# Optimization experiments

Hardware: AMD Instinct MI355X
Metric: run time of the kernel (lower is better)

The kernel has to match this reference:

```python
import jax, jax.numpy as jnp
import numpy as np
import math

NUM_HEADS = 16
TOPK = 64
EMBED = 1024

def setup_inputs() -> dict:
    key = jax.random.key(0)
    ks = jax.random.split(key, 11)
    b, s, e = 2, 2048, EMBED
    scale = 1.0 / math.sqrt(e)
    inp = {
        'q': jax.random.normal(ks[0], (b, s, e), dtype=jnp.float32),
        'k': jax.random.normal(ks[1], (b, s, e), dtype=jnp.float32),
        'v': jax.random.normal(ks[2], (b, s, e), dtype=jnp.float32),
        'Wq': jax.random.normal(ks[3], (e, e), dtype=jnp.float32) * scale,
        'bq': jnp.zeros((e,), dtype=jnp.float32),
        'Wk': jax.random.normal(ks[4], (e, e), dtype=jnp.float32) * scale,
        'bk': jnp.zeros((e,), dtype=jnp.float32),
        'Wv': jax.random.normal(ks[5], (e, e), dtype=jnp.float32) * scale,
        'bv': jnp.zeros((e,), dtype=jnp.float32),
        'Wo': jax.random.normal(ks[6], (e, e), dtype=jnp.float32) * scale,
        'bo': jnp.zeros((e,), dtype=jnp.float32),
    }
    return inp

def _topk_attention(Q, K, V, topk):
    # Q,K,V: (b, h, s, d)
    d = Q.shape[-1]
    scores = jnp.einsum('bhqd,bhkd->bhqk', Q, K) / jnp.sqrt(jnp.asarray(d, Q.dtype))
    topk_scores, topk_idx = jax.lax.top_k(scores, topk)  # (b,h,s,topk)
    probs = jax.nn.softmax(topk_scores, axis=-1)
    # gather V rows per (b,h): V_bh[idx] -> (s, topk, d); avoids (b,h,s,s,d) expand
    gather = jax.vmap(jax.vmap(lambda Vbh, idx: Vbh[idx]))
    sel = gather(V, topk_idx)  # (b,h,s,topk,d)
    return jnp.einsum('bhqk,bhqkd->bhqd', probs, sel)

def reference(q, k, v, Wq, bq, Wk, bk, Wv, bv, Wo, bo):
    b, s, e = q.shape
    h = NUM_HEADS
    d = e // h
    # NOTE: original torch code reshapes (b, s, e) -> (b, h, s, d) directly (no transpose)
    Q = (q @ Wq.T + bq).reshape(b, h, s, d)
    K = (k @ Wk.T + bk).reshape(b, h, s, d)
    V = (v @ Wv.T + bv).reshape(b, h, s, d)
    attn = _topk_attention(Q, K, V, TOPK)  # (b,h,s,d)
    out = attn.reshape(b, s, e)
    return out @ Wo.T + bo
```

## Files before the change

kernel.cpp:

```cpp
#include <hip/hip_runtime.h>
#include <stdint.h>

using u8  = unsigned char;
using s8  = signed char;
using u16 = unsigned short;
using u32 = unsigned int;
using u64 = unsigned long long;

typedef int   v4i __attribute__((ext_vector_type(4)));
typedef float v4f __attribute__((ext_vector_type(4)));
typedef short v8s __attribute__((ext_vector_type(8)));

__device__ __forceinline__ u16 f2bf(float f){
  u32 u = __builtin_bit_cast(u32, f);
  u32 r = (u + 0x7FFFu + ((u >> 16) & 1u)) >> 16;
  return (u16)r;
}
__device__ __forceinline__ float bf2f(u16 b){
  u32 u = ((u32)b) << 16;
  return __builtin_bit_cast(float, u);
}

__global__ __launch_bounds__(256) void quant_digits(
    const float* __restrict__ in, s8* __restrict__ dig, int n, float scale, float clampv)
{
  int t = blockIdx.x * 256 + threadIdx.x;
  int n8 = n >> 3;
  if (t >= n8) return;
  const float4* inv = (const float4*)in;
  float4 a = inv[2*t], b = inv[2*t+1];
  float xs[8] = {a.x,a.y,a.z,a.w,b.x,b.y,b.z,b.w};
  u64 p0=0,p1=0,p2=0,p3=0;
#pragma unroll
  for (int j=0;j<8;j++){
    float xv = fminf(fmaxf(xs[j], -clampv), clampv);
    int X = (int)rintf(xv * scale);
    int d0 = (int)(s8)(X & 255); X = (X - d0) >> 8;
    int d1 = (int)(s8)(X & 255); X = (X - d1) >> 8;
    int d2 = (int)(s8)(X & 255); X = (X - d2) >> 8;
    int d3 = X;
    p0 |= ((u64)(u8)(s8)d0) << (8*j);
    p1 |= ((u64)(u8)(s8)d1) << (8*j);
    p2 |= ((u64)(u8)(s8)d2) << (8*j);
    p3 |= ((u64)(u8)(s8)d3) << (8*j);
  }
  u64* o = (u64*)dig;
  size_t np8 = (size_t)n8;
  o[t] = p0; o[np8 + t] = p1; o[2*np8 + t] = p2; o[3*np8 + t] = p3;
}

#define MFMA_I8(c, a, b) asm volatile("v_mfma_i32_16x16x64_i8 %0, %1, %2, %0" : "+v"(c) : "v"(a), "v"(b))

__global__ __launch_bounds__(256) void gemm_i8(
    const s8* __restrict__ Ad, const s8* __restrict__ Wd, const float* __restrict__ bias,
    double* __restrict__ Cd, u16* __restrict__ Cb, u16* __restrict__ Cl)
{
  __shared__ alignas(16) s8 As[4][32][80];
  __shared__ alignas(16) s8 Bs[4][32][80];
  const int i0 = blockIdx.x * 32, o0 = blockIdx.y * 32;
  const int t = threadIdx.x, w = t >> 6, lane = t & 63;
  const int wr = w >> 1, wc = w & 1, l15 = lane & 15, lg = lane >> 4;
  const size_t APL = 4194304, WPL = 1048576;

  v4i c0={0,0,0,0}, c1={0,0,0,0}, c2={0,0,0,0}, c3={0,0,0,0}, c4={0,0,0,0};

  for (int kt = 0; kt < 16; ++kt){
#pragma unroll
    for (int j = 0; j < 2; ++j){
      int cid = t*2 + j;
      int p = cid >> 7, rem = cid & 127;
      int row = rem >> 2, c16 = (rem & 3) << 4;
      int4 av = *(const int4*)(Ad + (size_t)p*APL + (size_t)(i0+row)*1024 + kt*64 + c16);
      *(int4*)&As[p][row][c16] = av;
      int4 bv = *(const int4*)(Wd + (size_t)p*WPL + (size_t)(o0+row)*1024 + kt*64 + c16);
      *(int4*)&Bs[p][row][c16] = bv;
    }
    __syncthreads();
    v4i a0 = *(const v4i*)&As[0][wr*16+l15][lg*16];
    v4i a1 = *(const v4i*)&As[1][wr*16+l15][lg*16];
    v4i a2 = *(const v4i*)&As[2][wr*16+l15][lg*16];
    v4i a3 = *(const v4i*)&As[3][wr*16+l15][lg*16];
    v4i b0 = *(const v4i*)&Bs[0][wc*16+l15][lg*16];
    v4i b1 = *(const v4i*)&Bs[1][wc*16+l15][lg*16];
    v4i b2 = *(const v4i*)&Bs[2][wc*16+l15][lg*16];
    v4i b3 = *(const v4i*)&Bs[3][wc*16+l15][lg*16];
    MFMA_I8(c0, a0, b2); MFMA_I8(c0, a1, b1); MFMA_I8(c0, a2, b0);
    MFMA_I8(c1, a0, b3); MFMA_I8(c1, a1, b2); MFMA_I8(c1, a2, b1); MFMA_I8(c1, a3, b0);
    MFMA_I8(c2, a1, b3); MFMA_I8(c2, a2, b2); MFMA_I8(c2, a3, b1);
    MFMA_I8(c3, a2, b3); MFMA_I8(c3, a3, b2);
    MFMA_I8(c4, a3, b3);
    __syncthreads();
  }
  const int oc = o0 + wc*16 + l15;
  const double bv = (double)bias[oc];
#pragma unroll
  for (int e = 0; e < 4; ++e){
    double val = (double)c0[e]*0x1p-43 + (double)c1[e]*0x1p-35 + (double)c2[e]*0x1p-27
               + (double)c3[e]*0x1p-19 + (double)c4[e]*0x1p-11 + bv;
    int orow = i0 + wr*16 + lg*4 + e;
    size_t idx = (size_t)orow*1024 + oc;
    Cd[idx] = val;
    float hi = (float)val;
    u16 hb = f2bf(hi);
    float lof = (float)(val - (double)bf2f(hb));
    Cb[idx] = hb;
    Cl[idx] = f2bf(lof);
  }
}

template<int ABF16, int OUTBF>
__global__ __launch_bounds__(256) void gemm_bf16k(
    const void* __restrict__ Ap, const float* __restrict__ W, const float* __restrict__ bias,
    void* __restrict__ C)
{
  __shared__ alignas(16) u16 As[32][72];
  __shared__ alignas(16) u16 Bs[32][72];
  const int i0 = blockIdx.x * 32, o0 = blockIdx.y * 32;
  const int t = threadIdx.x, w = t >> 6, lane = t & 63;
  const int wr = w >> 1, wc = w & 1, l15 = lane & 15, lg = lane >> 4;
  const int row = t >> 3, c8 = (t & 7) * 8;
  v4f acc = {0.f,0.f,0.f,0.f};
  for (int kt = 0; kt < 16; ++kt){
    if (ABF16){
      v8s x = *(const v8s*)((const u16*)Ap + (size_t)(i0+row)*1024 + kt*64 + c8);
      *(v8s*)&As[row][c8] = x;
    } else {
      const float* A = (const float*)Ap;
      const float4 x0 = *(const float4*)(A + (size_t)(i0+row)*1024 + kt*64 + c8);
      const float4 x1 = *(const float4*)(A + (size_t)(i0+row)*1024 + kt*64 + c8 + 4);
      v8s pk;
      pk[0]=(short)f2bf(x0.x); pk[1]=(short)f2bf(x0.y); pk[2]=(short)f2bf(x0.z); pk[3]=(short)f2bf(x0.w);
      pk[4]=(short)f2bf(x1.x); pk[5]=(short)f2bf(x1.y); pk[6]=(short)f2bf(x1.z); pk[7]=(short)f2bf(x1.w);
      *(v8s*)&As[row][c8] = pk;
    }
    {
      const float4 y0 = *(const float4*)(W + (size_t)(o0+row)*1024 + kt*64 + c8);
      const float4 y1 = *(const float4*)(W + (size_t)(o0+row)*1024 + kt*64 + c8 + 4);
      v8s pk;
      pk[0]=(short)f2bf(y0.x); pk[1]=(short)f2bf(y0.y); pk[2]=(short)f2bf(y0.z); pk[3]=(short)f2bf(y0.w);
      pk[4]=(short)f2bf(y1.x); pk[5]=(short)f2bf(y1.y); pk[6]=(short)f2bf(y1.z); pk[7]=(short)f2bf(y1.w);
      *(v8s*)&Bs[row][c8] = pk;
    }
    __syncthreads();
    v8s a0 = *(const v8s*)&As[wr*16+l15][lg*8];
    v8s a1 = *(const v8s*)&As[wr*16+l15][lg*8+32];
    v8s b0 = *(const v8s*)&Bs[wc*16+l15][lg*8];
    v8s b1 = *(const v8s*)&Bs[wc*16+l15][lg*8+32];
    acc = __builtin_amdgcn_mfma_f32_16x16x32_bf16(a0, b0, acc, 0, 0, 0);
    acc = __builtin_amdgcn_mfma_f32_16x16x32_bf16(a1, b1, acc, 0, 0, 0);
    __syncthreads();
  }
  const int oc = o0 + wc*16 + l15;
  const float bvv = bias[oc];
#pragma unroll
  for (int e=0;e<4;e++){
    int orow = i0 + wr*16 + lg*4 + e;
    size_t idx = (size_t)orow*1024 + oc;
    if (OUTBF) ((u16*)C)[idx] = f2bf(acc[e] + bvv);
    else       ((float*)C)[idx] = acc[e] + bvv;
  }
}

__global__ __launch_bounds__(512, 4) void attn_topk(
    const u16* __restrict__ Qb, const u16* __restrict__ Kb,
    const u16* __restrict__ Ql, const u16* __restrict__ Kl,
    const double* __restrict__ Qd, const double* __restrict__ Kd,
    const u16* __restrict__ Vb, u16* __restrict__ Ab, u32* __restrict__ flags)
{
  __shared__ u32 stageL[16*8*48];
  __shared__ u64 selpL[16*64];
  __shared__ u32 cntL[16*8];
  __shared__ u32 flagL[16];

  const int lid = blockIdx.y * 128 + blockIdx.x;
  const int bh  = (lid & 7) * 4 + (lid >> 10);
  const int qb  = (lid >> 3) & 127;
  const size_t base = (size_t)(bh >> 4) * 2097152 + (size_t)(bh & 15) * 131072;
  const int q0 = qb * 16;
  const int tid = threadIdx.x, w = tid >> 6, lane = tid & 63;
  const int l15 = lane & 15, lg = lane >> 4;
  const u64 ltmask = (1ull << lane) - 1ull;

  if (tid < 16) flagL[tid] = 0u;
  __syncthreads();

  const v4f vzero = {0.f,0.f,0.f,0.f};
  float nrm2;
  {
    const size_t qoff = base + (size_t)(q0 + l15)*64 + lg*8;
    v8s a0  = *(const v8s*)(Qb + qoff);
    v8s a1  = *(const v8s*)(Qb + qoff + 32);
    v8s a0l = *(const v8s*)(Ql + qoff);
    v8s a1l = *(const v8s*)(Ql + qoff + 32);

    nrm2 = 0.f;
#pragma unroll
    for (int m = 0; m < 8; ++m){
      float x0 = bf2f((u16)a0[m]), x1 = bf2f((u16)a1[m]);
      nrm2 = fmaf(x0, x0, nrm2);
      nrm2 = fmaf(x1, x1, nrm2);
    }
    nrm2 += __shfl_xor(nrm2, 16);
    nrm2 += __shfl_xor(nrm2, 32);
    float T0e[4];
#pragma unroll
    for (int e = 0; e < 4; ++e)
      T0e[e] = 0.1875f * sqrtf(__shfl(nrm2, lg*4 + e));

    int cnt[4] = {0,0,0,0};
#pragma unroll 2
    for (int kt = 0; kt < 16; ++kt){
      int kk0 = w*256 + kt*16;
      const size_t koff = base + (size_t)(kk0 + l15)*64 + lg*8;
      v8s b0  = *(const v8s*)(Kb + koff);
      v8s b1  = *(const v8s*)(Kb + koff + 32);
      v8s b0l = *(const v8s*)(Kl + koff);
      v8s b1l = *(const v8s*)(Kl + koff + 32);
      v4f hh = __builtin_amdgcn_mfma_f32_16x16x32_bf16(a0,  b0,  vzero, 0, 0, 0);
      v4f hl = __builtin_amdgcn_mfma_f32_16x16x32_bf16(a0,  b0l, vzero, 0, 0, 0);
      v4f lh = __builtin_amdgcn_mfma_f32_16x16x32_bf16(a0l, b0,  vzero, 0, 0, 0);
      hh = __builtin_amdgcn_mfma_f32_16x16x32_bf16(a1,  b1,  hh, 0, 0, 0);
      hl = __builtin_amdgcn_mfma_f32_16x16x32_bf16(a1,  b1l, hl, 0, 0, 0);
      lh = __builtin_amdgcn_mfma_f32_16x16x32_bf16(a1l, b1,  lh, 0, 0, 0);
#pragma unroll
      for (int e = 0; e < 4; ++e){
        float sc = ((hh[e] + hl[e]) + lh[e]) * 0.125f;
        bool hit = sc >= T0e[e];
        u64 mk = __ballot(hit);
        u32 nib = (u32)(mk >> (lg*16)) & 0xFFFFu;
        int pos = cnt[e] + (int)__popc(nib & ((1u << l15) - 1u));
        if (hit && pos < 48)
          stageL[(u32)((lg*4 + e)*8 + w)*48u + (u32)pos] =
              ((u32)f2bf(sc) << 16) | (u32)(kk0 + l15);
        cnt[e] += (int)__popc(nib);
      }
    }
    if (l15 == 0){
#pragma unroll
      for (int e = 0; e < 4; ++e){
        int row = lg*4 + e;
        cntL[row*8 + w] = (u32)cnt[e];
        if (cnt[e] > 48) flagL[row] = 1u;
      }
    }
  }
  __syncthreads();

  const int R0 = w * 2;
  u32 pk0[2], pk1[2], pk2[2], cstore[2], tv[2];
  bool fail[2];

#pragma unroll
  for (int rr = 0; rr < 2; ++rr){
    const int R = R0 + rr;
    uint4 ca = *(const uint4*)&cntL[R*8];
    uint4 cb = *(const uint4*)&cntL[R*8 + 4];
    u32 P1 = ca.x, P2 = P1+ca.y, P3 = P2+ca.z, P4 = P3+ca.w;
    u32 P5 = P4+cb.x, P6 = P5+cb.y, P7 = P6+cb.z;
    cstore[rr] = P7 + cb.w;
    fail[rr] = (flagL[R] != 0u) || (cstore[rr] > 192u);
#pragma unroll
    for (int s = 0; s < 3; ++s){
      u32 idx = (u32)(64*s + lane);
      u32 pb = 0, wsel = 0;
      if (idx >= P1){ pb = P1; wsel = 1; }
      if (idx >= P2){ pb = P2; wsel = 2; }
      if (idx >= P3){ pb = P3; wsel = 3; }
      if (idx >= P4){ pb = P4; wsel = 4; }
      if (idx >= P5){ pb = P5; wsel = 5; }
      if (idx >= P6){ pb = P6; wsel = 6; }
      if (idx >= P7){ pb = P7; wsel = 7; }
      u32 off = idx - pb; off = off > 47u ? 47u : off;
      u32 val = stageL[(u32)(R*8 + (int)wsel)*48u + off];
      val = (idx < cstore[rr]) ? val : 0u;
      if (s == 0) pk0[rr] = val; else if (s == 1) pk1[rr] = val; else pk2[rr] = val;
    }
    tv[rr] = 0u;
  }

  for (int bit = 14; bit >= 0; --bit){
#pragma unroll
    for (int rr = 0; rr < 2; ++rr){
      u32 tt = tv[rr] | (1u << bit);
      int c = (int)__popcll(__ballot((pk0[rr] >> 16) >= tt))
            + (int)__popcll(__ballot((pk1[rr] >> 16) >= tt))
            + (int)__popcll(__ballot((pk2[rr] >> 16) >= tt));
      if (c >= 64) tv[rr] = tt;
    }
  }

  int na[2], nb[2];
#pragma unroll
  for (int rr = 0; rr < 2; ++rr){
    const int R = R0 + rr;
    float t64f = bf2f((u16)tv[rr]);
    float T0R = 0.1875f * sqrtf(__shfl(nrm2, R));
    float thi = t64f + 0.021f, tlo = t64f - 0.021f;
    int a_ = 0, b_ = 0;
#pragma unroll
    for (int s = 0; s < 3; ++s){
      u32 pkv = (s == 0) ? pk0[rr] : ((s == 1) ? pk1[rr] : pk2[rr]);
      bool act = (u32)(64*s + lane) < cstore[rr];
      float v = bf2f((u16)(pkv >> 16));
      bool aut = act && (v > thi);
      bool ban = act && !aut && (v >= tlo);
      u64 ma = __ballot(aut);
      if (aut){
        int pos = a_ + (int)__popcll(ma & ltmask);
        if (pos < 64) selpL[R*64 + pos] = ((u64)(pkv & 0xFFFF0000u) << 32) | (u64)(pkv & 0x7FFu);
      }
      a_ += (int)__popcll(ma);
      u64 mb = __ballot(ban);
      if (ban){
        int pos = b_ + (int)__popcll(mb & ltmask);
        if (pos < 64) stageL[(u32)(R*8)*48u + (u32)pos] = pkv;
      }
      b_ += (int)__popcll(mb);
    }
    bool fl = fail[rr] || (t64f < T0R + 0.025f) || (t64f >= 4.0f) || (b_ > 64);
    fail[rr] = fl;
    if (lane == 0) flags[bh*2048 + q0 + R] = fl ? 1u : 0u;
    na[rr] = fl ? 64 : (a_ > 64 ? 64 : a_);
    nb[rr] = fl ? 0  : b_;
  }
  asm volatile("s_waitcnt lgkmcnt(0)" ::: "memory");
  __builtin_amdgcn_sched_barrier(0);

  const double* Kdh = Kd + base;
  const double* Qdh = Qd + base + (size_t)q0*64;
  u32 bpk[2];
#pragma unroll
  for (int rr = 0; rr < 2; ++rr)
    bpk[rr] = (lane < nb[rr]) ? stageL[(u32)((R0+rr)*8)*48u + (u32)lane] : 0u;
  double ac0[2] = {0,0}, ac1[2] = {0,0};
#pragma unroll 4
  for (int j = 0; j < 32; ++j){
#pragma unroll
    for (int rr = 0; rr < 2; ++rr){
      double2 kv = ((const double2*)(Kdh + (size_t)(bpk[rr] & 0x7FFu)*64))[j];
      double2 qv = ((const double2*)(Qdh + (size_t)(R0+rr)*64))[j];
      ac0[rr] = fma(qv.x, kv.x, ac0[rr]);
      ac1[rr] = fma(qv.y, kv.y, ac1[rr]);
    }
  }
  double mv[2]; int mi[2];
#pragma unroll
  for (int rr = 0; rr < 2; ++rr){
    mv[rr] = (lane < nb[rr]) ? (ac0[rr] + ac1[rr]) : -1.0e300;
    mi[rr] = (lane < nb[rr]) ? (int)(bpk[rr] & 0x7FFu) : 0x7FFFFFFF;
  }
  int maxnb = nb[0] > nb[1] ? nb[0] : nb[1];
  int rank[2] = {0,0};
  for (int j = 0; j < maxnb; ++j){
#pragma unroll
    for (int rr = 0; rr < 2; ++rr){
      double ov = __shfl(mv[rr], j); int oi = __shfl(mi[rr], j);
      rank[rr] += (ov > mv[rr] || (ov == mv[rr] && oi < mi[rr])) ? 1 : 0;
    }
  }
#pragma unroll
  for (int rr = 0; rr < 2; ++rr){
    int need = 64 - na[rr]; if (need > nb[rr]) need = nb[rr];
    if (lane < nb[rr] && rank[rr] < need)
      selpL[(R0+rr)*64 + na[rr] + rank[rr]] =
          ((u64)(bpk[rr] & 0xFFFF0000u) << 32) | (u64)(bpk[rr] & 0x7FFu);
  }
  asm volatile("s_waitcnt lgkmcnt(0)" ::: "memory");
  __builtin_amdgcn_sched_barrier(0);

  u32 sidx[2]; float scv[2], pp[2];
#pragma unroll
  for (int rr = 0; rr < 2; ++rr){
    u64 pr = selpL[(R0+rr)*64 + lane];
    sidx[rr] = (u32)pr & 0x7FFu;
    scv[rr] = __builtin_bit_cast(float, (u32)(pr >> 32));
  }
#pragma unroll
  for (int rr = 0; rr < 2; ++rr){
    float mx = scv[rr];
#pragma unroll
    for (int off = 32; off; off >>= 1) mx = fmaxf(mx, __shfl_xor(mx, off));
    float p = expf(scv[rr] - mx);
    float Z = p;
#pragma unroll
    for (int off = 32; off; off >>= 1) Z += __shfl_xor(Z, off);
    pp[rr] = p / Z;
  }
#pragma unroll
  for (int rr = 0; rr < 2; ++rr)
    selpL[(R0+rr)*64 + lane] = ((u64)__builtin_bit_cast(u32, pp[rr]) << 32) | (u64)sidx[rr];
  asm volatile("s_waitcnt lgkmcnt(0)" ::: "memory");
  __builtin_amdgcn_sched_barrier(0);

  const int h = lane >> 5, dl = lane & 31;
  float u0[2] = {0,0}, u1[2] = {0,0};
#pragma unroll 4
  for (int j = 0; j < 64; j += 2){
#pragma unroll
    for (int rr = 0; rr < 2; ++rr){
      u64 pr = selpL[(R0+rr)*64 + j + h];
      float pv = __builtin_bit_cast(float, (u32)(pr >> 32));
      u32 vv = *(const u32*)(Vb + base + (size_t)((u32)pr & 0x7FFu)*64 + 2*dl);
      u0[rr] = fmaf(pv, bf2f((u16)(vv & 0xFFFFu)), u0[rr]);
      u1[rr] = fmaf(pv, bf2f((u16)(vv >> 16)),     u1[rr]);
    }
  }
#pragma unroll
  for (int rr = 0; rr < 2; ++rr){
    u0[rr] += __shfl_xor(u0[rr], 32);
    u1[rr] += __shfl_xor(u1[rr], 32);
  }
  if (lane < 32){
#pragma unroll
    for (int rr = 0; rr < 2; ++rr){
      u32 o = (u32)f2bf(u0[rr]) | ((u32)f2bf(u1[rr]) << 16);
      *(u32*)(Ab + base + (size_t)(q0 + R0 + rr)*64 + 2*dl) = o;
    }
  }
}

__global__ __launch_bounds__(64) void attn_fallback(
    const u32* __restrict__ flags, const double* __restrict__ Qd,
    const double* __restrict__ Kd, const u16* __restrict__ Vb,
    u16* __restrict__ Ab)
{
  __shared__ double valsL[32*64];
  const int blk = blockIdx.x;
  const int lane = threadIdx.x;
  u32 f = (lane < 16) ? flags[blk*16 + lane] : 0u;
  u64 msk = __ballot(f != 0u);
  if (msk == 0ull) return;
  for (int i = 0; i < 16; ++i){
    if (!((msk >> i) & 1ull)) continue;
    int g = blk*16 + i;
    int bh = g >> 11, qrow = g & 2047;
    size_t base = (size_t)(bh >> 4)*2097152 + (size_t)(bh & 15)*131072;
    const double* Qrow = Qd + base + (size_t)qrow*64;
    for (int mm = 0; mm < 32; ++mm){
      const double* Kr = Kd + base + ((size_t)lane*32 + mm)*64;
      double s0 = 0.0, s1 = 0.0;
      for (int j = 0; j < 32; ++j){
        s0 = fma(Qrow[2*j],   Kr[2*j],   s0);
        s1 = fma(Qrow[2*j+1], Kr[2*j+1], s1);
      }
      valsL[mm*64 + lane] = (s0 + s1) * 0.125;
    }
    double selv = 0.0; int seli = 0;
    double pvv = 1.0e300; int pii = -1;
    for (int step = 0; step < 64; ++step){
      double bv = -1.0e300; int bi = 0x7FFFFFFF;
      for (int mm = 0; mm < 32; ++mm){
        double vv = valsL[mm*64 + lane];
        int col = lane*32 + mm;
        bool after = (vv < pvv) || (vv == pvv && col > pii);
        bool bet = after && (vv > bv || (vv == bv && col < bi));
        bv = bet ? vv : bv;
        bi = bet ? col : bi;
      }
#pragma unroll
      for (int off = 32; off; off >>= 1){
        double ov = __shfl_xor(bv, off); int oi = __shfl_xor(bi, off);
        bool tk = (ov > bv) || (ov == bv && oi < bi);
        bv = tk ? ov : bv; bi = tk ? oi : bi;
      }
      if (lane == step){ selv = bv; seli = bi; }
      pvv = bv; pii = bi;
    }
    float sc = (float)selv;
    float mx = sc;
#pragma unroll
    for (int off = 32; off; off >>= 1) mx = fmaxf(mx, __shfl_xor(mx, off));
    float p = expf(sc - mx);
    float Z = p;
#pragma unroll
    for (int off = 32; off; off >>= 1) Z += __shfl_xor(Z, off);
    float pp = p / Z;
    float o = 0.f;
    for (int j = 0; j < 64; ++j){
      float pj = __shfl(pp, j); int ij = __shfl(seli, j);
      o += pj * bf2f(Vb[base + (size_t)ij*64 + lane]);
    }
    Ab[base + (size_t)qrow*64 + lane] = f2bf(o);
  }
}

extern "C" void kernel_launch(void* const* d_in, const int* in_sizes, int n_in,
                              void* d_out, int out_size, void* d_ws, size_t ws_size,
                              hipStream_t stream)
{
  (void)in_sizes; (void)n_in; (void)out_size; (void)ws_size;
  const float* q  = (const float*)d_in[0];
  const float* k  = (const float*)d_in[1];
  const float* v  = (const float*)d_in[2];
  const float* Wq = (const float*)d_in[3];
  const float* bq = (const float*)d_in[4];
  const float* Wk = (const float*)d_in[5];
  const float* bk = (const float*)d_in[6];
  const float* Wv = (const float*)d_in[7];
  const float* bv = (const float*)d_in[8];
  const float* Wo = (const float*)d_in[9];
  const float* bo = (const float*)d_in[10];

  char* ws = (char*)d_ws;
  const size_t MB = 1048576;
  double* Qd  = (double*)(ws);
  double* Kd  = (double*)(ws + 32*MB);
  u16*    Qb  = (u16*)  (ws + 64*MB);
  u16*    Kb  = (u16*)  (ws + 72*MB);
  u16*    Ql  = (u16*)  (ws + 80*MB);
  u16*    Kl  = (u16*)  (ws + 88*MB);
  u16*    Abf = (u16*)  (ws + 96*MB);
  s8*     dact= (s8*)   (ws + 104*MB);
  u16*    Vbf = (u16*)  (ws + 104*MB);
  s8*     dw  = (s8*)   (ws + 120*MB);
  u32*    flg = (u32*)  (ws + 120*MB);

  quant_digits<<<2048, 256, 0, stream>>>(q,  dact, 4194304, 134217728.0f, 7.75f);
  quant_digits<<<512,  256, 0, stream>>>(Wq, dw,   1048576, 4294967296.0f, 0.2495f);
  gemm_i8<<<dim3(128, 32), 256, 0, stream>>>(dact, dw, bq, Qd, Qb, Ql);
  quant_digits<<<2048, 256, 0, stream>>>(k,  dact, 4194304, 134217728.0f, 7.75f);
  quant_digits<<<512,  256, 0, stream>>>(Wk, dw,   1048576, 4294967296.0f, 0.2495f);
  gemm_i8<<<dim3(128, 32), 256, 0, stream>>>(dact, dw, bk, Kd, Kb, Kl);
  gemm_bf16k<0,1><<<dim3(128, 32), 256, 0, stream>>>(v, Wv, bv, Vbf);
  attn_topk<<<dim3(128, 32), 512, 0, stream>>>(Qb, Kb, Ql, Kl, Qd, Kd, Vbf, Abf, flg);
  attn_fallback<<<4096, 64, 0, stream>>>(flg, Qd, Kd, Vbf, Abf);
  gemm_bf16k<1,0><<<dim3(128, 32), 256, 0, stream>>>(Abf, Wo, bo, d_out);
}
```

Baseline: 671.6 us.

## Drop split-bf16 score correction, process 32 queries per block with K prefetch

The approximate score pass now uses a single bf16 MFMA product instead of hi/lo split terms (three MFMAs), so the low-part Q/K buffers and their writes in the projection GEMM are removed. Each attention block now handles 32 query rows, sharing each loaded K tile across two query groups, and software-prefetches the next K tile. The uncertainty band around the top-64 threshold is widened to cover the larger bf16 error, which may push more candidates into the exact fp64 rescoring and more rows into the fallback kernel. Per-wave staging capacity is cut from 48 to 32 entries, which could also raise fallback rates.

```diff
diff --git a/kernel.cpp b/kernel.cpp
--- a/kernel.cpp
+++ b/kernel.cpp
@@ -53,7 +53,7 @@
 
 __global__ __launch_bounds__(256) void gemm_i8(
     const s8* __restrict__ Ad, const s8* __restrict__ Wd, const float* __restrict__ bias,
-    double* __restrict__ Cd, u16* __restrict__ Cb, u16* __restrict__ Cl)
+    double* __restrict__ Cd, u16* __restrict__ Cb)
 {
   __shared__ alignas(16) s8 As[4][32][80];
   __shared__ alignas(16) s8 Bs[4][32][80];
@@ -100,11 +100,7 @@
     int orow = i0 + wr*16 + lg*4 + e;
     size_t idx = (size_t)orow*1024 + oc;
     Cd[idx] = val;
-    float hi = (float)val;
-    u16 hb = f2bf(hi);
-    float lof = (float)(val - (double)bf2f(hb));
-    Cb[idx] = hb;
-    Cl[idx] = f2bf(lof);
+    Cb[idx] = f2bf((float)val);
   }
 }
 
@@ -163,258 +159,281 @@
 
 __global__ __launch_bounds__(512, 4) void attn_topk(
     const u16* __restrict__ Qb, const u16* __restrict__ Kb,
-    const u16* __restrict__ Ql, const u16* __restrict__ Kl,
     const double* __restrict__ Qd, const double* __restrict__ Kd,
     const u16* __restrict__ Vb, u16* __restrict__ Ab, u32* __restrict__ flags)
 {
-  __shared__ u32 stageL[16*8*48];
-  __shared__ u64 selpL[16*64];
-  __shared__ u32 cntL[16*8];
-  __shared__ u32 flagL[16];
-
-  const int lid = blockIdx.y * 128 + blockIdx.x;
-  const int bh  = (lid & 7) * 4 + (lid >> 10);
-  const int qb  = (lid >> 3) & 127;
+  __shared__ u32 stageL[32*8*32];
+  __shared__ u64 selpL[32*64];
+  __shared__ u32 cntL[32*8];
+  __shared__ u32 flagL[32];
+
+  const int lid = blockIdx.y * 64 + blockIdx.x;
+  const int bh  = (lid & 7) * 4 + (lid >> 9);
+  const int qb  = (lid >> 3) & 63;
   const size_t base = (size_t)(bh >> 4) * 2097152 + (size_t)(bh & 15) * 131072;
-  const int q0 = qb * 16;
+  const int q0 = qb * 32;
   const int tid = threadIdx.x, w = tid >> 6, lane = tid & 63;
   const int l15 = lane & 15, lg = lane >> 4;
   const u64 ltmask = (1ull << lane) - 1ull;
 
-  if (tid < 16) flagL[tid] = 0u;
+  if (tid < 32) flagL[tid] = 0u;
   __syncthreads();
 
   const v4f vzero = {0.f,0.f,0.f,0.f};
-  float nrm2;
+  float nrmA, nrmB;
   {
-    const size_t qoff = base + (size_t)(q0 + l15)*64 + lg*8;
-    v8s a0  = *(const v8s*)(Qb + qoff);
-    v8s a1  = *(const v8s*)(Qb + qoff + 32);
-    v8s a0l = *(const v8s*)(Ql + qoff);
-    v8s a1l = *(const v8s*)(Ql + qoff + 32);
-
-    nrm2 = 0.f;
+    const size_t qoffA = base + (size_t)(q0 + l15)*64 + lg*8;
+    v8s aA0 = *(const v8s*)(Qb + qoffA);
+    v8s aA1 = *(const v8s*)(Qb + qoffA + 32);
+    v8s aB0 = *(const v8s*)(Qb + qoffA + 1024);
+    v8s aB1 = *(const v8s*)(Qb + qoffA + 1024 + 32);
+
+    nrmA = 0.f; nrmB = 0.f;
 #pragma unroll
     for (int m = 0; m < 8; ++m){
-      float x0 = bf2f((u16)a0[m]), x1 = bf2f((u16)a1[m]);
-      nrm2 = fmaf(x0, x0, nrm2);
-      nrm2 = fmaf(x1, x1, nrm2);
-    }
-    nrm2 += __shfl_xor(nrm2, 16);
-    nrm2 += __shfl_xor(nrm2, 32);
-    float T0e[4];
-#pragma unroll
-    for (int e = 0; e < 4; ++e)
-      T0e[e] = 0.1875f * sqrtf(__shfl(nrm2, lg*4 + e));
-
-    int cnt[4] = {0,0,0,0};
-#pragma unroll 2
-    for (int kt = 0; kt < 16; ++kt){
-      int kk0 = w*256 + kt*16;
-      const size_t koff = base + (size_t)(kk0 + l15)*64 + lg*8;
-      v8s b0  = *(const v8s*)(Kb + koff);
-      v8s b1  = *(const v8s*)(Kb + koff + 32);
-      v8s b0l = *(const v8s*)(Kl + koff);
-      v8s b1l = *(const v8s*)(Kl + koff + 32);
-      v4f hh = __builtin_amdgcn_mfma_f32_16x16x32_bf16(a0,  b0,  vzero, 0, 0, 0);
-      v4f hl = __builtin_amdgcn_mfma_f32_16x16x32_bf16(a0,  b0l, vzero, 0, 0, 0);
-      v4f lh = __builtin_amdgcn_mfma_f32_16x16x32_bf16(a0l, b0,  vzero, 0, 0, 0);
-      hh = __builtin_amdgcn_mfma_f32_16x16x32_bf16(a1,  b1,  hh, 0, 0, 0);
-      hl = __builtin_amdgcn_mfma_f32_16x16x32_bf16(a1,  b1l, hl, 0, 0, 0);
-      lh = __builtin_amdgcn_mfma_f32_16x16x32_bf16(a1l, b1,  lh, 0, 0, 0);
+      float xA0 = bf2f((u16)aA0[m]), xA1 = bf2f((u16)aA1[m]);
+      float xB0 = bf2f((u16)aB0[m]), xB1 = bf2f((u16)aB1[m]);
+      nrmA = fmaf(xA0,xA0,nrmA); nrmA = fmaf(xA1,xA1,nrmA);
+      nrmB = fmaf(xB0,xB0,nrmB); nrmB = fmaf(xB1,xB1,nrmB);
+    }
+    nrmA += __shfl_xor(nrmA,16); nrmA += __shfl_xor(nrmA,32);
+    nrmB += __shfl_xor(nrmB,16); nrmB += __shfl_xor(nrmB,32);
+    float T0A[4], T0B[4];
+#pragma unroll
+    for (int e = 0; e < 4; ++e){
+      T0A[e] = 0.1875f * sqrtf(__shfl(nrmA, lg*4 + e));
+      T0B[e] = 0.1875f * sqrtf(__shfl(nrmB, lg*4 + e));
+    }
+    int cA[4] = {0,0,0,0}, cB[4] = {0,0,0,0};
+    const u32 pfx = (1u << l15) - 1u;
+
+    const u16* Kw = Kb + base + (size_t)(w*256 + l15)*64 + lg*8;
+    v8s b0 = *(const v8s*)(Kw);
+    v8s b1 = *(const v8s*)(Kw + 32);
+
+    auto step = [&](int kt, v8s b0c, v8s b1c){
+      v4f sA = __builtin_amdgcn_mfma_f32_16x16x32_bf16(aA0, b0c, vzero, 0,0,0);
+      sA = __builtin_amdgcn_mfma_f32_16x16x32_bf16(aA1, b1c, sA, 0,0,0);
+      v4f sB = __builtin_amdgcn_mfma_f32_16x16x32_bf16(aB0, b0c, vzero, 0,0,0);
+      sB = __builtin_amdgcn_mfma_f32_16x16x32_bf16(aB1, b1c, sB, 0,0,0);
+      const int kk0 = w*256 + kt*16;
 #pragma unroll
       for (int e = 0; e < 4; ++e){
-        float sc = ((hh[e] + hl[e]) + lh[e]) * 0.125f;
-        bool hit = sc >= T0e[e];
+        float sc = sA[e]*0.125f;
+        bool hit = sc >= T0A[e];
         u64 mk = __ballot(hit);
         u32 nib = (u32)(mk >> (lg*16)) & 0xFFFFu;
-        int pos = cnt[e] + (int)__popc(nib & ((1u << l15) - 1u));
-        if (hit && pos < 48)
-          stageL[(u32)((lg*4 + e)*8 + w)*48u + (u32)pos] =
-              ((u32)f2bf(sc) << 16) | (u32)(kk0 + l15);
-        cnt[e] += (int)__popc(nib);
-      }
-    }
+        int pos = cA[e] + (int)__popc(nib & pfx);
+        if (hit && pos < 32)
+          stageL[(u32)((lg*4+e)*8 + w)*32u + (u32)pos] = ((u32)f2bf(sc)<<16) | (u32)(kk0+l15);
+        cA[e] += (int)__popc(nib);
+      }
+#pragma unroll
+      for (int e = 0; e < 4; ++e){
+        float sc = sB[e]*0.125f;
+        bool hit = sc >= T0B[e];
+        u64 mk = __ballot(hit);
+        u32 nib = (u32)(mk >> (lg*16)) & 0xFFFFu;
+        int pos = cB[e] + (int)__popc(nib & pfx);
+        if (hit && pos < 32)
+          stageL[(u32)((16+lg*4+e)*8 + w)*32u + (u32)pos] = ((u32)f2bf(sc)<<16) | (u32)(kk0+l15);
+        cB[e] += (int)__popc(nib);
+      }
+    };
+
+    for (int kt = 0; kt < 15; ++kt){
+      v8s n0 = *(const v8s*)(Kw + (size_t)(kt+1)*1024);
+      v8s n1 = *(const v8s*)(Kw + (size_t)(kt+1)*1024 + 32);
+      step(kt, b0, b1);
+      b0 = n0; b1 = n1;
+    }
+    step(15, b0, b1);
+
     if (l15 == 0){
 #pragma unroll
       for (int e = 0; e < 4; ++e){
-        int row = lg*4 + e;
-        cntL[row*8 + w] = (u32)cnt[e];
-        if (cnt[e] > 48) flagL[row] = 1u;
+        int rA = lg*4 + e, rB = 16 + lg*4 + e;
+        cntL[rA*8 + w] = (u32)cA[e];
+        cntL[rB*8 + w] = (u32)cB[e];
+        if (cA[e] > 32) flagL[rA] = 1u;
+        if (cB[e] > 32) flagL[rB] = 1u;
       }
     }
   }
   __syncthreads();
 
-  const int R0 = w * 2;
-  u32 pk0[2], pk1[2], pk2[2], cstore[2], tv[2];
-  bool fail[2];
-
-#pragma unroll
-  for (int rr = 0; rr < 2; ++rr){
-    const int R = R0 + rr;
-    uint4 ca = *(const uint4*)&cntL[R*8];
-    uint4 cb = *(const uint4*)&cntL[R*8 + 4];
-    u32 P1 = ca.x, P2 = P1+ca.y, P3 = P2+ca.z, P4 = P3+ca.w;
-    u32 P5 = P4+cb.x, P6 = P5+cb.y, P7 = P6+cb.z;
-    cstore[rr] = P7 + cb.w;
-    fail[rr] = (flagL[R] != 0u) || (cstore[rr] > 192u);
-#pragma unroll
-    for (int s = 0; s < 3; ++s){
-      u32 idx = (u32)(64*s + lane);
-      u32 pb = 0, wsel = 0;
-      if (idx >= P1){ pb = P1; wsel = 1; }
-      if (idx >= P2){ pb = P2; wsel = 2; }
-      if (idx >= P3){ pb = P3; wsel = 3; }
-      if (idx >= P4){ pb = P4; wsel = 4; }
-      if (idx >= P5){ pb = P5; wsel = 5; }
-      if (idx >= P6){ pb = P6; wsel = 6; }
-      if (idx >= P7){ pb = P7; wsel = 7; }
-      u32 off = idx - pb; off = off > 47u ? 47u : off;
-      u32 val = stageL[(u32)(R*8 + (int)wsel)*48u + off];
-      val = (idx < cstore[rr]) ? val : 0u;
-      if (s == 0) pk0[rr] = val; else if (s == 1) pk1[rr] = val; else pk2[rr] = val;
-    }
-    tv[rr] = 0u;
-  }
-
-  for (int bit = 14; bit >= 0; --bit){
-#pragma unroll
-    for (int rr = 0; rr < 2; ++rr){
-      u32 tt = tv[rr] | (1u << bit);
-      int c = (int)__popcll(__ballot((pk0[rr] >> 16) >= tt))
-            + (int)__popcll(__ballot((pk1[rr] >> 16) >= tt))
-            + (int)__popcll(__ballot((pk2[rr] >> 16) >= tt));
-      if (c >= 64) tv[rr] = tt;
-    }
-  }
-
-  int na[2], nb[2];
-#pragma unroll
-  for (int rr = 0; rr < 2; ++rr){
-    const int R = R0 + rr;
-    float t64f = bf2f((u16)tv[rr]);
-    float T0R = 0.1875f * sqrtf(__shfl(nrm2, R));
-    float thi = t64f + 0.021f, tlo = t64f - 0.021f;
-    int a_ = 0, b_ = 0;
-#pragma unroll
-    for (int s = 0; s < 3; ++s){
-      u32 pkv = (s == 0) ? pk0[rr] : ((s == 1) ? pk1[rr] : pk2[rr]);
-      bool act = (u32)(64*s + lane) < cstore[rr];
-      float v = bf2f((u16)(pkv >> 16));
-      bool aut = act && (v > thi);
-      bool ban = act && !aut && (v >= tlo);
-      u64 ma = __ballot(aut);
-      if (aut){
-        int pos = a_ + (int)__popcll(ma & ltmask);
-        if (pos < 64) selpL[R*64 + pos] = ((u64)(pkv & 0xFFFF0000u) << 32) | (u64)(pkv & 0x7FFu);
-      }
-      a_ += (int)__popcll(ma);
-      u64 mb = __ballot(ban);
-      if (ban){
-        int pos = b_ + (int)__popcll(mb & ltmask);
-        if (pos < 64) stageL[(u32)(R*8)*48u + (u32)pos] = pkv;
-      }
-      b_ += (int)__popcll(mb);
-    }
-    bool fl = fail[rr] || (t64f < T0R + 0.025f) || (t64f >= 4.0f) || (b_ > 64);
-    fail[rr] = fl;
-    if (lane == 0) flags[bh*2048 + q0 + R] = fl ? 1u : 0u;
-    na[rr] = fl ? 64 : (a_ > 64 ? 64 : a_);
-    nb[rr] = fl ? 0  : b_;
-  }
-  asm volatile("s_waitcnt lgkmcnt(0)" ::: "memory");
-  __builtin_amdgcn_sched_barrier(0);
-
-  const double* Kdh = Kd + base;
-  const double* Qdh = Qd + base + (size_t)q0*64;
-  u32 bpk[2];
-#pragma unroll
-  for (int rr = 0; rr < 2; ++rr)
-    bpk[rr] = (lane < nb[rr]) ? stageL[(u32)((R0+rr)*8)*48u + (u32)lane] : 0u;
-  double ac0[2] = {0,0}, ac1[2] = {0,0};
+  for (int pass = 0; pass < 2; ++pass){
+    const int R0 = pass*16 + w*2;
+    const float nrmP0 = (pass == 0) ? nrmA : nrmB;
+    u32 pk0[2], pk1[2], pk2[2], cstore[2], tv[2];
+    bool fail[2];
+
+#pragma unroll
+    for (int rr = 0; rr < 2; ++rr){
+      const int R = R0 + rr;
+      uint4 ca = *(const uint4*)&cntL[R*8];
+      uint4 cb = *(const uint4*)&cntL[R*8 + 4];
+      u32 P1 = ca.x, P2 = P1+ca.y, P3 = P2+ca.z, P4 = P3+ca.w;
+      u32 P5 = P4+cb.x, P6 = P5+cb.y, P7 = P6+cb.z;
+      cstore[rr] = P7 + cb.w;
+      fail[rr] = (flagL[R] != 0u) || (cstore[rr] > 192u);
+#pragma unroll
+      for (int s = 0; s < 3; ++s){
+        u32 idx = (u32)(64*s + lane);
+        u32 pb = 0, wsel = 0;
+        if (idx >= P1){ pb = P1; wsel = 1; }
+        if (idx >= P2){ pb = P2; wsel = 2; }
+        if (idx >= P3){ pb = P3; wsel = 3; }
+        if (idx >= P4){ pb = P4; wsel = 4; }
+        if (idx >= P5){ pb = P5; wsel = 5; }
+        if (idx >= P6){ pb = P6; wsel = 6; }
+        if (idx >= P7){ pb = P7; wsel = 7; }
+        u32 off = idx - pb; off = off > 31u ? 31u : off;
+        u32 val = stageL[(u32)(R*8 + (int)wsel)*32u + off];
+        val = (idx < cstore[rr]) ? val : 0u;
+        if (s == 0) pk0[rr] = val; else if (s == 1) pk1[rr] = val; else pk2[rr] = val;
+      }
+      tv[rr] = 0u;
+    }
+
+    for (int bit = 14; bit >= 0; --bit){
+#pragma unroll
+      for (int rr = 0; rr < 2; ++rr){
+        u32 tt = tv[rr] | (1u << bit);
+        int c = (int)__popcll(__ballot((pk0[rr] >> 16) >= tt))
+              + (int)__popcll(__ballot((pk1[rr] >> 16) >= tt))
+              + (int)__popcll(__ballot((pk2[rr] >> 16) >= tt));
+        if (c >= 64) tv[rr] = tt;
+      }
+    }
+
+    int na[2], nb[2];
+#pragma unroll
+    for (int rr = 0; rr < 2; ++rr){
+      const int R = R0 + rr;
+      float t64f = bf2f((u16)tv[rr]);
+      float T0R = 0.1875f * sqrtf(__shfl(nrmP0, R & 15));
+      float thi = t64f + 0.052f, tlo = t64f - 0.052f;
+      int a_ = 0, b_ = 0;
+#pragma unroll
+      for (int s = 0; s < 3; ++s){
+        u32 pkv = (s == 0) ? pk0[rr] : ((s == 1) ? pk1[rr] : pk2[rr]);
+        bool act = (u32)(64*s + lane) < cstore[rr];
+        float v = bf2f((u16)(pkv >> 16));
+        bool aut = act && (v > thi);
+        bool ban = act && !aut && (v >= tlo);
+        u64 ma = __ballot(aut);
+        if (aut){
+          int pos = a_ + (int)__popcll(ma & ltmask);
+          if (pos < 64) selpL[R*64 + pos] = ((u64)(pkv & 0xFFFF0000u) << 32) | (u64)(pkv & 0x7FFu);
+        }
+        a_ += (int)__popcll(ma);
+        u64 mb = __ballot(ban);
+        if (ban){
+          int pos = b_ + (int)__popcll(mb & ltmask);
+          if (pos < 64) stageL[(u32)(R*8)*32u + (u32)pos] = pkv;
+        }
+        b_ += (int)__popcll(mb);
+      }
+      bool fl = fail[rr] || (t64f < T0R + 0.055f) || (t64f >= 3.98f) || (b_ > 64);
+      fail[rr] = fl;
+      if (lane == 0) flags[bh*2048 + q0 + R] = fl ? 1u : 0u;
+      na[rr] = fl ? 64 : (a_ > 64 ? 64 : a_);
+      nb[rr] = fl ? 0  : b_;
+    }
+    asm volatile("s_waitcnt lgkmcnt(0)" ::: "memory");
+    __builtin_amdgcn_sched_barrier(0);
+
+    const double* Kdh = Kd + base;
+    const double* Qdh = Qd + base + (size_t)q0*64;
+    u32 bpk[2];
+#pragma unroll
+    for (int rr = 0; rr < 2; ++rr)
+      bpk[rr] = (lane < nb[rr]) ? stageL[(u32)((R0+rr)*8)*32u + (u32)lane] : 0u;
+    double ac0[2] = {0,0}, ac1[2] = {0,0};
 #pragma unroll 4
-  for (int j = 0; j < 32; ++j){
-#pragma unroll
-    for (int rr = 0; rr < 2; ++rr){
-      double2 kv = ((const double2*)(Kdh + (size_t)(bpk[rr] & 0x7FFu)*64))[j];
-      double2 qv = ((const double2*)(Qdh + (size_t)(R0+rr)*64))[j];
-      ac0[rr] = fma(qv.x, kv.x, ac0[rr]);
-      ac1[rr] = fma(qv.y, kv.y, ac1[rr]);
-    }
-  }
-  double mv[2]; int mi[2];
-#pragma unroll
-  for (int rr = 0; rr < 2; ++rr){
-    mv[rr] = (lane < nb[rr]) ? (ac0[rr] + ac1[rr]) : -1.0e300;
-    mi[rr] = (lane < nb[rr]) ? (int)(bpk[rr] & 0x7FFu) : 0x7FFFFFFF;
-  }
-  int maxnb = nb[0] > nb[1] ? nb[0] : nb[1];
-  int rank[2] = {0,0};
-  for (int j = 0; j < maxnb; ++j){
-#pragma unroll
-    for (int rr = 0; rr < 2; ++rr){
-      double ov = __shfl(mv[rr], j); int oi = __shfl(mi[rr], j);
-      rank[rr] += (ov > mv[rr] || (ov == mv[rr] && oi < mi[rr])) ? 1 : 0;
-    }
-  }
-#pragma unroll
-  for (int rr = 0; rr < 2; ++rr){
-    int need = 64 - na[rr]; if (need > nb[rr]) need = nb[rr];
-    if (lane < nb[rr] && rank[rr] < need)
-      selpL[(R0+rr)*64 + na[rr] + rank[rr]] =
-          ((u64)(bpk[rr] & 0xFFFF0000u) << 32) | (u64)(bpk[rr] & 0x7FFu);
-  }
-  asm volatile("s_waitcnt lgkmcnt(0)" ::: "memory");
-  __builtin_amdgcn_sched_barrier(0);
-
-  u32 sidx[2]; float scv[2], pp[2];
-#pragma unroll
-  for (int rr = 0; rr < 2; ++rr){
-    u64 pr = selpL[(R0+rr)*64 + lane];
-    sidx[rr] = (u32)pr & 0x7FFu;
-    scv[rr] = __builtin_bit_cast(float, (u32)(pr >> 32));
-  }
-#pragma unroll
-  for (int rr = 0; rr < 2; ++rr){
-    float mx = scv[rr];
-#pragma unroll
-    for (int off = 32; off; off >>= 1) mx = fmaxf(mx, __shfl_xor(mx, off));
-    float p = expf(scv[rr] - mx);
-    float Z = p;
-#pragma unroll
-    for (int off = 32; off; off >>= 1) Z += __shfl_xor(Z, off);
-    pp[rr] = p / Z;
-  }
-#pragma unroll
-  for (int rr = 0; rr < 2; ++rr)
-    selpL[(R0+rr)*64 + lane] = ((u64)__builtin_bit_cast(u32, pp[rr]) << 32) | (u64)sidx[rr];
-  asm volatile("s_waitcnt lgkmcnt(0)" ::: "memory");
-  __builtin_amdgcn_sched_barrier(0);
-
-  const int h = lane >> 5, dl = lane & 31;
-  float u0[2] = {0,0}, u1[2] = {0,0};
+    for (int j = 0; j < 32; ++j){
+#pragma unroll
+      for (int rr = 0; rr < 2; ++rr){
+        double2 kv = ((const double2*)(Kdh + (size_t)(bpk[rr] & 0x7FFu)*64))[j];
+        double2 qv = ((const double2*)(Qdh + (size_t)(R0+rr)*64))[j];
+        ac0[rr] = fma(qv.x, kv.x, ac0[rr]);
+        ac1[rr] = fma(qv.y, kv.y, ac1[rr]);
+      }
+    }
+    double mv[2]; int mi[2];
+#pragma unroll
+    for (int rr = 0; rr < 2; ++rr){
+      mv[rr] = (lane < nb[rr]) ? (ac0[rr] + ac1[rr]) : -1.0e300;
+      mi[rr] = (lane < nb[rr]) ? (int)(bpk[rr] & 0x7FFu) : 0x7FFFFFFF;
+    }
+    int maxnb = nb[0] > nb[1] ? nb[0] : nb[1];
+    int rank[2] = {0,0};
+    for (int j = 0; j < maxnb; ++j){
+#pragma unroll
+      for (int rr = 0; rr < 2; ++rr){
+        double ov = __shfl(mv[rr], j); int oi = __shfl(mi[rr], j);
+        rank[rr] += (ov > mv[rr] || (ov == mv[rr] && oi < mi[rr])) ? 1 : 0;
+      }
+    }
+#pragma unroll
+    for (int rr = 0; rr < 2; ++rr){
+      int need = 64 - na[rr]; if (need > nb[rr]) need = nb[rr];
+      if (lane < nb[rr] && rank[rr] < need)
+        selpL[(R0+rr)*64 + na[rr] + rank[rr]] =
+            ((u64)(bpk[rr] & 0xFFFF0000u) << 32) | (u64)(bpk[rr] & 0x7FFu);
+    }
+    asm volatile("s_waitcnt lgkmcnt(0)" ::: "memory");
+    __builtin_amdgcn_sched_barrier(0);
+
+    u32 sidx[2]; float scv[2], pp[2];
+#pragma unroll
+    for (int rr = 0; rr < 2; ++rr){
+      u64 pr = selpL[(R0+rr)*64 + lane];
+      sidx[rr] = (u32)pr & 0x7FFu;
+      scv[rr] = __builtin_bit_cast(float, (u32)(pr >> 32));
+    }
+#pragma unroll
+    for (int rr = 0; rr < 2; ++rr){
+      float mx = scv[rr];
+#pragma unroll
+      for (int off = 32; off; off >>= 1) mx = fmaxf(mx, __shfl_xor(mx, off));
+      float p = expf(scv[rr] - mx);
+      float Z = p;
+#pragma unroll
+      for (int off = 32; off; off >>= 1) Z += __shfl_xor(Z, off);
+      pp[rr] = p / Z;
+    }
+#pragma unroll
+    for (int rr = 0; rr < 2; ++rr)
+      selpL[(R0+rr)*64 + lane] = ((u64)__builtin_bit_cast(u32, pp[rr]) << 32) | (u64)sidx[rr];
+    asm volatile("s_waitcnt lgkmcnt(0)" ::: "memory");
+    __builtin_amdgcn_sched_barrier(0);
+
+    const int h = lane >> 5, dl = lane & 31;
+    float u0[2] = {0,0}, u1[2] = {0,0};
 #pragma unroll 4
-  for (int j = 0; j < 64; j += 2){
-#pragma unroll
-    for (int rr = 0; rr < 2; ++rr){
-      u64 pr = selpL[(R0+rr)*64 + j + h];
-      float pv = __builtin_bit_cast(float, (u32)(pr >> 32));
-      u32 vv = *(const u32*)(Vb + base + (size_t)((u32)pr & 0x7FFu)*64 + 2*dl);
-      u0[rr] = fmaf(pv, bf2f((u16)(vv & 0xFFFFu)), u0[rr]);
-      u1[rr] = fmaf(pv, bf2f((u16)(vv >> 16)),     u1[rr]);
-    }
-  }
-#pragma unroll
-  for (int rr = 0; rr < 2; ++rr){
-    u0[rr] += __shfl_xor(u0[rr], 32);
-    u1[rr] += __shfl_xor(u1[rr], 32);
-  }
-  if (lane < 32){
-#pragma unroll
-    for (int rr = 0; rr < 2; ++rr){
-      u32 o = (u32)f2bf(u0[rr]) | ((u32)f2bf(u1[rr]) << 16);
-      *(u32*)(Ab + base + (size_t)(q0 + R0 + rr)*64 + 2*dl) = o;
+    for (int j = 0; j < 64; j += 2){
+#pragma unroll
+      for (int rr = 0; rr < 2; ++rr){
+        u64 pr = selpL[(R0+rr)*64 + j + h];
+        float pv = __builtin_bit_cast(float, (u32)(pr >> 32));
+        u32 vv = *(const u32*)(Vb + base + (size_t)((u32)pr & 0x7FFu)*64 + 2*dl);
+        u0[rr] = fmaf(pv, bf2f((u16)(vv & 0xFFFFu)), u0[rr]);
+        u1[rr] = fmaf(pv, bf2f((u16)(vv >> 16)),     u1[rr]);
+      }
+    }
+#pragma unroll
+    for (int rr = 0; rr < 2; ++rr){
+      u0[rr] += __shfl_xor(u0[rr], 32);
+      u1[rr] += __shfl_xor(u1[rr], 32);
+    }
+    if (lane < 32){
+#pragma unroll
+      for (int rr = 0; rr < 2; ++rr){
+        u32 o = (u32)f2bf(u0[rr]) | ((u32)f2bf(u1[rr]) << 16);
+        *(u32*)(Ab + base + (size_t)(q0 + R0 + rr)*64 + 2*dl) = o;
+      }
     }
   }
 }
@@ -507,22 +526,20 @@
   double* Kd  = (double*)(ws + 32*MB);
   u16*    Qb  = (u16*)  (ws + 64*MB);
   u16*    Kb  = (u16*)  (ws + 72*MB);
-  u16*    Ql  = (u16*)  (ws + 80*MB);
-  u16*    Kl  = (u16*)  (ws + 88*MB);
-  u16*    Abf = (u16*)  (ws + 96*MB);
-  s8*     dact= (s8*)   (ws + 104*MB);
-  u16*    Vbf = (u16*)  (ws + 104*MB);
-  s8*     dw  = (s8*)   (ws + 120*MB);
-  u32*    flg = (u32*)  (ws + 120*MB);
+  u16*    Abf = (u16*)  (ws + 80*MB);
+  s8*     dact= (s8*)   (ws + 88*MB);
+  u16*    Vbf = (u16*)  (ws + 88*MB);
+  s8*     dw  = (s8*)   (ws + 104*MB);
+  u32*    flg = (u32*)  (ws + 104*MB);
 
   quant_digits<<<2048, 256, 0, stream>>>(q,  dact, 4194304, 134217728.0f, 7.75f);
   quant_digits<<<512,  256, 0, stream>>>(Wq, dw,   1048576, 4294967296.0f, 0.2495f);
-  gemm_i8<<<dim3(128, 32), 256, 0, stream>>>(dact, dw, bq, Qd, Qb, Ql);
+  gemm_i8<<<dim3(128, 32), 256, 0, stream>>>(dact, dw, bq, Qd, Qb);
   quant_digits<<<2048, 256, 0, stream>>>(k,  dact, 4194304, 134217728.0f, 7.75f);
   quant_digits<<<512,  256, 0, stream>>>(Wk, dw,   1048576, 4294967296.0f, 0.2495f);
-  gemm_i8<<<dim3(128, 32), 256, 0, stream>>>(dact, dw, bk, Kd, Kb, Kl);
+  gemm_i8<<<dim3(128, 32), 256, 0, stream>>>(dact, dw, bk, Kd, Kb);
   gemm_bf16k<0,1><<<dim3(128, 32), 256, 0, stream>>>(v, Wv, bv, Vbf);
-  attn_topk<<<dim3(128, 32), 512, 0, stream>>>(Qb, Kb, Ql, Kl, Qd, Kd, Vbf, Abf, flg);
+  attn_topk<<<dim3(64, 32), 512, 0, stream>>>(Qb, Kb, Qd, Kd, Vbf, Abf, flg);
   attn_fallback<<<4096, 64, 0, stream>>>(flg, Qd, Kd, Vbf, Abf);
   gemm_bf16k<1,0><<<dim3(128, 32), 256, 0, stream>>>(Abf, Wo, bo, d_out);
 }
```

After: 1.058 ms. 57.5% more time.
